# Performance work log

Measured on AMD Instinct MI355X. Metric: run time of the kernel, lower is better.

Reference implementation:

```python
import jax, jax.numpy as jnp
import numpy as np

NUM_BITS = 4
C0, RES0 = 8, 2048
C1, RES1 = 8, 1024
N = 2097152


def _quant_consts(num_bits):
    n = 1 << num_bits
    q = 1.0 / n
    lo = -((n - 1) * 0.5) * q
    hi = n * 0.5 * q
    return n, q, lo, hi


def fake_quant(x, num_bits=NUM_BITS):
    # hard quant path: codes from detached x, dequantize (no grad, matches torch .detach())
    n, q, lo, _ = _quant_consts(num_bits)
    codes = jnp.clip(jnp.round((jax.lax.stop_gradient(x) - lo) / q), 0, n - 1)
    return codes * q + lo


def grid_sample_bilinear(img, gx, gy):
    # img: [C,H,W]; gx,gy: [N] in [-1,1]; align_corners=False, zeros padding
    C, H, W = img.shape
    ix = (gx + 1.0) * 0.5 * W - 0.5
    iy = (gy + 1.0) * 0.5 * H - 0.5
    x0 = jnp.floor(ix)
    y0 = jnp.floor(iy)
    x1, y1 = x0 + 1.0, y0 + 1.0
    wx1 = ix - x0
    wx0 = 1.0 - wx1
    wy1 = iy - y0
    wy0 = 1.0 - wy1

    def tap(xi, yi, w):
        valid = ((xi >= 0) & (xi <= W - 1) & (yi >= 0) & (yi <= H - 1)).astype(img.dtype)
        xc = jnp.clip(xi, 0, W - 1).astype(jnp.int32)
        yc = jnp.clip(yi, 0, H - 1).astype(jnp.int32)
        return img[:, yc, xc] * (valid * w)  # [C,N]

    out = (tap(x0, y0, wx0 * wy0) + tap(x1, y0, wx1 * wy0)
           + tap(x0, y1, wx0 * wy1) + tap(x1, y1, wx1 * wy1))
    return out.T  # [N,C]


def setup_inputs() -> dict:
    key = jax.random.key(0)
    k1, k2, k3 = jax.random.split(key, 3)
    _, _, lo, hi = _quant_consts(NUM_BITS)
    scale = (hi - lo) * 0.25
    uv = jax.random.uniform(k1, (N, 2), dtype=jnp.float32)
    g0 = jax.random.uniform(k2, (1, C0, RES0, RES0), dtype=jnp.float32, minval=-scale, maxval=scale)
    g1 = jax.random.uniform(k3, (1, C1, RES1, RES1), dtype=jnp.float32, minval=-scale, maxval=scale)
    return {"uv": uv, "g0": g0, "g1": g1}


def reference(uv, g0, g1):
    res0 = g0.shape[-1]
    g0q = fake_quant(g0)
    g1q = fake_quant(g1)

    # high-res G0: 4-neighbor gather + concat
    pos = uv * res0 - 0.5
    x0 = jnp.clip(jnp.floor(pos[:, 0]), 0, res0 - 2).astype(jnp.int32)
    y0 = jnp.clip(jnp.floor(pos[:, 1]), 0, res0 - 2).astype(jnp.int32)
    x1, y1 = x0 + 1, y0 + 1
    plane = jnp.transpose(g0q[0], (1, 2, 0))  # [res0, res0, c0]
    feat0 = jnp.concatenate([plane[y0, x0], plane[y0, x1],
                             plane[y1, x0], plane[y1, x1]], axis=-1)  # [N, 4*c0]

    # low-res G1: bilinear grid_sample
    grid = uv * 2.0 - 1.0
    feat1 = grid_sample_bilinear(g1q[0], grid[:, 0], grid[:, 1])  # [N, c1]

    return jnp.concatenate([feat0, feat1], axis=-1)  # [N, 4*c0 + c1]
```

## Files before the change

kernel.cpp:

```cpp
#include <hip/hip_runtime.h>
#include <stdint.h>

#define RES0 2048
#define RES1 1024
#define HW0 (RES0 * RES0)
#define HW1 (RES1 * RES1)

#define QLO (-0.46875f)
#define QSC (0.0625f)

__device__ __forceinline__ uint32_t qcode(float x) {
    float t = (x - QLO) * 16.0f;
    float r = rintf(t);
    r = fminf(fmaxf(r, 0.0f), 15.0f);
    return (uint32_t)(int)r;
}

__device__ __forceinline__ float dq(uint32_t packed, int c) {
    return (float)((packed >> (4 * c)) & 15u) * QSC + QLO;
}

__global__ __launch_bounds__(256) void pack_both_kernel(
    const float4* __restrict__ g0, const float4* __restrict__ g1,
    uint4* __restrict__ p0, uint4* __restrict__ p1)
{
    const int i = blockIdx.x * 256 + threadIdx.x;
    const int n0 = HW0 / 4;
    const int n1 = HW1 / 4;
    if (i < n0) {
        uint4 r = make_uint4(0u, 0u, 0u, 0u);
#pragma unroll
        for (int c = 0; c < 8; ++c) {
            float4 v = g0[(size_t)c * n0 + i];
            r.x |= qcode(v.x) << (4 * c);
            r.y |= qcode(v.y) << (4 * c);
            r.z |= qcode(v.z) << (4 * c);
            r.w |= qcode(v.w) << (4 * c);
        }
        p0[i] = r;
    } else {
        const int j = i - n0;
        if (j < n1) {
            uint4 r = make_uint4(0u, 0u, 0u, 0u);
#pragma unroll
            for (int c = 0; c < 8; ++c) {
                float4 v = g1[(size_t)c * n1 + j];
                r.x |= qcode(v.x) << (4 * c);
                r.y |= qcode(v.y) << (4 * c);
                r.z |= qcode(v.z) << (4 * c);
                r.w |= qcode(v.w) << (4 * c);
            }
            p1[j] = r;
        }
    }
}

__global__ __launch_bounds__(256) void sample_kernel(
    const float2* __restrict__ uv,
    const uint32_t* __restrict__ p0,
    const uint32_t* __restrict__ p1,
    float* __restrict__ out, int n)
{
#pragma clang fp contract(off)
    const int i = blockIdx.x * 256 + threadIdx.x;
    if (i >= n) return;
    const float2 u = uv[i];

    float o[40];

    float px = u.x * 2048.0f; px = px - 0.5f;
    float py = u.y * 2048.0f; py = py - 0.5f;
    float fx = fminf(fmaxf(floorf(px), 0.0f), 2046.0f);
    float fy = fminf(fmaxf(floorf(py), 0.0f), 2046.0f);
    const int x0 = (int)fx;
    const int y0 = (int)fy;
    const uint32_t* row = p0 + y0 * RES0 + x0;
    const uint32_t t00 = row[0];
    const uint32_t t01 = row[1];
    const uint32_t t10 = row[RES0];
    const uint32_t t11 = row[RES0 + 1];
#pragma unroll
    for (int c = 0; c < 8; ++c) {
        o[c]      = dq(t00, c);
        o[8 + c]  = dq(t01, c);
        o[16 + c] = dq(t10, c);
        o[24 + c] = dq(t11, c);
    }

    const float gx = u.x * 2.0f - 1.0f;
    const float gy = u.y * 2.0f - 1.0f;
    float ix = (gx + 1.0f) * 0.5f; ix = ix * 1024.0f; ix = ix - 0.5f;
    float iy = (gy + 1.0f) * 0.5f; iy = iy * 1024.0f; iy = iy - 0.5f;
    const float x0f = floorf(ix);
    const float y0f = floorf(iy);
    const float wx1 = ix - x0f;
    const float wy1 = iy - y0f;
    const float wx0 = 1.0f - wx1;
    const float wy0 = 1.0f - wy1;
    const int jx0 = (int)x0f, jy0 = (int)y0f;
    const int jx1 = jx0 + 1,  jy1 = jy0 + 1;
    const bool vx0 = (jx0 >= 0) && (jx0 <= RES1 - 1);
    const bool vx1 = (jx1 >= 0) && (jx1 <= RES1 - 1);
    const bool vy0 = (jy0 >= 0) && (jy0 <= RES1 - 1);
    const bool vy1 = (jy1 >= 0) && (jy1 <= RES1 - 1);
    const int cx0 = min(max(jx0, 0), RES1 - 1);
    const int cx1 = min(max(jx1, 0), RES1 - 1);
    const int cy0 = min(max(jy0, 0), RES1 - 1);
    const int cy1 = min(max(jy1, 0), RES1 - 1);
    const uint32_t s00 = p1[cy0 * RES1 + cx0];
    const uint32_t s10 = p1[cy0 * RES1 + cx1];
    const uint32_t s01 = p1[cy1 * RES1 + cx0];
    const uint32_t s11 = p1[cy1 * RES1 + cx1];
    const float w00 = (vx0 && vy0) ? wx0 * wy0 : 0.0f;
    const float w10 = (vx1 && vy0) ? wx1 * wy0 : 0.0f;
    const float w01 = (vx0 && vy1) ? wx0 * wy1 : 0.0f;
    const float w11 = (vx1 && vy1) ? wx1 * wy1 : 0.0f;
#pragma unroll
    for (int c = 0; c < 8; ++c) {
        float a = dq(s00, c) * w00 + dq(s10, c) * w10;
        a = a + dq(s01, c) * w01;
        a = a + dq(s11, c) * w11;
        o[32 + c] = a;
    }

    float4* dst = (float4*)(out + (size_t)i * 40);
#pragma unroll
    for (int k = 0; k < 10; ++k) {
        dst[k] = make_float4(o[4 * k], o[4 * k + 1], o[4 * k + 2], o[4 * k + 3]);
    }
}

__device__ __forceinline__ float fq1(float x) {
    float r = fminf(fmaxf(rintf((x - QLO) * 16.0f), 0.0f), 15.0f);
    return r * QSC + QLO;
}

__global__ __launch_bounds__(256) void sample_direct_kernel(
    const float2* __restrict__ uv,
    const float* __restrict__ g0,
    const float* __restrict__ g1,
    float* __restrict__ out, int n)
{
#pragma clang fp contract(off)
    const int i = blockIdx.x * 256 + threadIdx.x;
    if (i >= n) return;
    const float2 u = uv[i];
    float o[40];

    float px = u.x * 2048.0f; px = px - 0.5f;
    float py = u.y * 2048.0f; py = py - 0.5f;
    const int x0 = (int)fminf(fmaxf(floorf(px), 0.0f), 2046.0f);
    const int y0 = (int)fminf(fmaxf(floorf(py), 0.0f), 2046.0f);
#pragma unroll
    for (int c = 0; c < 8; ++c) {
        const float* pl = g0 + (size_t)c * HW0;
        o[c]      = fq1(pl[y0 * RES0 + x0]);
        o[8 + c]  = fq1(pl[y0 * RES0 + x0 + 1]);
        o[16 + c] = fq1(pl[(y0 + 1) * RES0 + x0]);
        o[24 + c] = fq1(pl[(y0 + 1) * RES0 + x0 + 1]);
    }

    const float gx = u.x * 2.0f - 1.0f;
    const float gy = u.y * 2.0f - 1.0f;
    float ix = (gx + 1.0f) * 0.5f; ix = ix * 1024.0f; ix = ix - 0.5f;
    float iy = (gy + 1.0f) * 0.5f; iy = iy * 1024.0f; iy = iy - 0.5f;
    const float x0f = floorf(ix), y0f = floorf(iy);
    const float wx1 = ix - x0f, wy1 = iy - y0f;
    const float wx0 = 1.0f - wx1, wy0 = 1.0f - wy1;
    const int jx0 = (int)x0f, jy0 = (int)y0f;
    const int jx1 = jx0 + 1, jy1 = jy0 + 1;
    const bool vx0 = (jx0 >= 0) && (jx0 < RES1);
    const bool vx1 = (jx1 >= 0) && (jx1 < RES1);
    const bool vy0 = (jy0 >= 0) && (jy0 < RES1);
    const bool vy1 = (jy1 >= 0) && (jy1 < RES1);
    const int cx0 = min(max(jx0, 0), RES1 - 1);
    const int cx1 = min(max(jx1, 0), RES1 - 1);
    const int cy0 = min(max(jy0, 0), RES1 - 1);
    const int cy1 = min(max(jy1, 0), RES1 - 1);
    const float w00 = (vx0 && vy0) ? wx0 * wy0 : 0.0f;
    const float w10 = (vx1 && vy0) ? wx1 * wy0 : 0.0f;
    const float w01 = (vx0 && vy1) ? wx0 * wy1 : 0.0f;
    const float w11 = (vx1 && vy1) ? wx1 * wy1 : 0.0f;
#pragma unroll
    for (int c = 0; c < 8; ++c) {
        const float* pl = g1 + (size_t)c * HW1;
        float a = fq1(pl[cy0 * RES1 + cx0]) * w00 + fq1(pl[cy0 * RES1 + cx1]) * w10;
        a = a + fq1(pl[cy1 * RES1 + cx0]) * w01;
        a = a + fq1(pl[cy1 * RES1 + cx1]) * w11;
        o[32 + c] = a;
    }

    float4* dst = (float4*)(out + (size_t)i * 40);
#pragma unroll
    for (int k = 0; k < 10; ++k) {
        dst[k] = make_float4(o[4 * k], o[4 * k + 1], o[4 * k + 2], o[4 * k + 3]);
    }
}

extern "C" void kernel_launch(void* const* d_in, const int* in_sizes, int n_in,
                              void* d_out, int out_size, void* d_ws, size_t ws_size,
                              hipStream_t stream)
{
    const float* uv = (const float*)d_in[0];
    const float* g0 = (const float*)d_in[1];
    const float* g1 = (const float*)d_in[2];
    float* out = (float*)d_out;
    const int n = in_sizes[0] / 2;

    const size_t need = (size_t)(HW0 + HW1) * sizeof(uint32_t);
    if (ws_size >= need) {
        uint32_t* p0 = (uint32_t*)d_ws;
        uint32_t* p1 = p0 + HW0;
        const int pack_threads = (HW0 + HW1) / 4;
        pack_both_kernel<<<(pack_threads + 255) / 256, 256, 0, stream>>>(
            (const float4*)g0, (const float4*)g1, (uint4*)p0, (uint4*)p1);
        sample_kernel<<<(n + 255) / 256, 256, 0, stream>>>(
            (const float2*)uv, p0, p1, out, n);
    } else {
        sample_direct_kernel<<<(n + 255) / 256, 256, 0, stream>>>(
            (const float2*)uv, g0, g1, out, n);
    }
}
```

Measured before the change: 595.1 us.

## Pack grids into 2x2 texel quads and stage output through LDS for coalesced stores

The packed 4-bit grids are re-laid out so each uint4 holds a 2x2 block of texels, so the four bilinear neighbours of a sample fall within one to four adjacent 16-byte quads, which is meant to improve cache-line locality of the gathers. The sample kernel also writes its 40-float rows into shared memory (padded to 11 float4 per row) and then stores them block-cooperatively, so consecutive threads write consecutive float4s instead of each thread writing a 160-byte strided row. This adds a block barrier, extra LDS traffic and more per-fetch select logic, and the pack kernel now reads float2 with row-pair strides.

```diff
diff --git a/kernel.cpp b/kernel.cpp
--- a/kernel.cpp
+++ b/kernel.cpp
@@ -5,6 +5,8 @@
 #define RES1 1024
 #define HW0 (RES0 * RES0)
 #define HW1 (RES1 * RES1)
+#define NQ0 ((RES0 / 2) * (RES0 / 2))
+#define NQ1 ((RES1 / 2) * (RES1 / 2))
 
 #define QLO (-0.46875f)
 #define QSC (0.0625f)
@@ -20,113 +22,142 @@
     return (float)((packed >> (4 * c)) & 15u) * QSC + QLO;
 }
 
-__global__ __launch_bounds__(256) void pack_both_kernel(
-    const float4* __restrict__ g0, const float4* __restrict__ g1,
-    uint4* __restrict__ p0, uint4* __restrict__ p1)
+__device__ __forceinline__ uint32_t texel_fetch(const uint4* __restrict__ map,
+                                                int pitch_q, int x, int y) {
+    uint4 Q = map[(y >> 1) * pitch_q + (x >> 1)];
+    uint32_t lo = (x & 1) ? Q.y : Q.x;
+    uint32_t hi = (x & 1) ? Q.w : Q.z;
+    return (y & 1) ? hi : lo;
+}
+
+__global__ __launch_bounds__(256) void pack_quads_kernel(
+    const float2* __restrict__ g0, const float2* __restrict__ g1,
+    uint4* __restrict__ q0, uint4* __restrict__ q1)
 {
     const int i = blockIdx.x * 256 + threadIdx.x;
-    const int n0 = HW0 / 4;
-    const int n1 = HW1 / 4;
-    if (i < n0) {
+    if (i < NQ0) {
+        const int qx = i & 1023;
+        const int qy = i >> 10;
         uint4 r = make_uint4(0u, 0u, 0u, 0u);
 #pragma unroll
         for (int c = 0; c < 8; ++c) {
-            float4 v = g0[(size_t)c * n0 + i];
-            r.x |= qcode(v.x) << (4 * c);
-            r.y |= qcode(v.y) << (4 * c);
-            r.z |= qcode(v.z) << (4 * c);
-            r.w |= qcode(v.w) << (4 * c);
-        }
-        p0[i] = r;
+            float2 r0 = g0[(size_t)c * (HW0 / 2) + (size_t)(2 * qy) * 1024 + qx];
+            float2 r1 = g0[(size_t)c * (HW0 / 2) + (size_t)(2 * qy + 1) * 1024 + qx];
+            r.x |= qcode(r0.x) << (4 * c);
+            r.y |= qcode(r0.y) << (4 * c);
+            r.z |= qcode(r1.x) << (4 * c);
+            r.w |= qcode(r1.y) << (4 * c);
+        }
+        q0[i] = r;
     } else {
-        const int j = i - n0;
-        if (j < n1) {
+        const int j = i - NQ0;
+        if (j < NQ1) {
+            const int qx = j & 511;
+            const int qy = j >> 9;
             uint4 r = make_uint4(0u, 0u, 0u, 0u);
 #pragma unroll
             for (int c = 0; c < 8; ++c) {
-                float4 v = g1[(size_t)c * n1 + j];
-                r.x |= qcode(v.x) << (4 * c);
-                r.y |= qcode(v.y) << (4 * c);
-                r.z |= qcode(v.z) << (4 * c);
-                r.w |= qcode(v.w) << (4 * c);
+                float2 r0 = g1[(size_t)c * (HW1 / 2) + (size_t)(2 * qy) * 512 + qx];
+                float2 r1 = g1[(size_t)c * (HW1 / 2) + (size_t)(2 * qy + 1) * 512 + qx];
+                r.x |= qcode(r0.x) << (4 * c);
+                r.y |= qcode(r0.y) << (4 * c);
+                r.z |= qcode(r1.x) << (4 * c);
+                r.w |= qcode(r1.y) << (4 * c);
             }
-            p1[j] = r;
+            q1[j] = r;
         }
     }
 }
 
 __global__ __launch_bounds__(256) void sample_kernel(
     const float2* __restrict__ uv,
-    const uint32_t* __restrict__ p0,
-    const uint32_t* __restrict__ p1,
+    const uint4* __restrict__ q0,
+    const uint4* __restrict__ q1,
     float* __restrict__ out, int n)
 {
 #pragma clang fp contract(off)
-    const int i = blockIdx.x * 256 + threadIdx.x;
-    if (i >= n) return;
-    const float2 u = uv[i];
-
-    float o[40];
-
-    float px = u.x * 2048.0f; px = px - 0.5f;
-    float py = u.y * 2048.0f; py = py - 0.5f;
-    float fx = fminf(fmaxf(floorf(px), 0.0f), 2046.0f);
-    float fy = fminf(fmaxf(floorf(py), 0.0f), 2046.0f);
-    const int x0 = (int)fx;
-    const int y0 = (int)fy;
-    const uint32_t* row = p0 + y0 * RES0 + x0;
-    const uint32_t t00 = row[0];
-    const uint32_t t01 = row[1];
-    const uint32_t t10 = row[RES0];
-    const uint32_t t11 = row[RES0 + 1];
-#pragma unroll
-    for (int c = 0; c < 8; ++c) {
-        o[c]      = dq(t00, c);
-        o[8 + c]  = dq(t01, c);
-        o[16 + c] = dq(t10, c);
-        o[24 + c] = dq(t11, c);
-    }
-
-    const float gx = u.x * 2.0f - 1.0f;
-    const float gy = u.y * 2.0f - 1.0f;
-    float ix = (gx + 1.0f) * 0.5f; ix = ix * 1024.0f; ix = ix - 0.5f;
-    float iy = (gy + 1.0f) * 0.5f; iy = iy * 1024.0f; iy = iy - 0.5f;
-    const float x0f = floorf(ix);
-    const float y0f = floorf(iy);
-    const float wx1 = ix - x0f;
-    const float wy1 = iy - y0f;
-    const float wx0 = 1.0f - wx1;
-    const float wy0 = 1.0f - wy1;
-    const int jx0 = (int)x0f, jy0 = (int)y0f;
-    const int jx1 = jx0 + 1,  jy1 = jy0 + 1;
-    const bool vx0 = (jx0 >= 0) && (jx0 <= RES1 - 1);
-    const bool vx1 = (jx1 >= 0) && (jx1 <= RES1 - 1);
-    const bool vy0 = (jy0 >= 0) && (jy0 <= RES1 - 1);
-    const bool vy1 = (jy1 >= 0) && (jy1 <= RES1 - 1);
-    const int cx0 = min(max(jx0, 0), RES1 - 1);
-    const int cx1 = min(max(jx1, 0), RES1 - 1);
-    const int cy0 = min(max(jy0, 0), RES1 - 1);
-    const int cy1 = min(max(jy1, 0), RES1 - 1);
-    const uint32_t s00 = p1[cy0 * RES1 + cx0];
-    const uint32_t s10 = p1[cy0 * RES1 + cx1];
-    const uint32_t s01 = p1[cy1 * RES1 + cx0];
-    const uint32_t s11 = p1[cy1 * RES1 + cx1];
-    const float w00 = (vx0 && vy0) ? wx0 * wy0 : 0.0f;
-    const float w10 = (vx1 && vy0) ? wx1 * wy0 : 0.0f;
-    const float w01 = (vx0 && vy1) ? wx0 * wy1 : 0.0f;
-    const float w11 = (vx1 && vy1) ? wx1 * wy1 : 0.0f;
-#pragma unroll
-    for (int c = 0; c < 8; ++c) {
-        float a = dq(s00, c) * w00 + dq(s10, c) * w10;
-        a = a + dq(s01, c) * w01;
-        a = a + dq(s11, c) * w11;
-        o[32 + c] = a;
-    }
-
-    float4* dst = (float4*)(out + (size_t)i * 40);
-#pragma unroll
-    for (int k = 0; k < 10; ++k) {
-        dst[k] = make_float4(o[4 * k], o[4 * k + 1], o[4 * k + 2], o[4 * k + 3]);
+    __shared__ float4 lds4[256 * 11];
+    const int t = threadIdx.x;
+    const int i = blockIdx.x * 256 + t;
+
+    if (i < n) {
+        const float2 u = uv[i];
+
+        float px = u.x * 2048.0f; px = px - 0.5f;
+        float py = u.y * 2048.0f; py = py - 0.5f;
+        float fx = fminf(fmaxf(floorf(px), 0.0f), 2046.0f);
+        float fy = fminf(fmaxf(floorf(py), 0.0f), 2046.0f);
+        const int x0 = (int)fx;
+        const int y0 = (int)fy;
+        const uint32_t t00 = texel_fetch(q0, 1024, x0,     y0);
+        const uint32_t t01 = texel_fetch(q0, 1024, x0 + 1, y0);
+        const uint32_t t10 = texel_fetch(q0, 1024, x0,     y0 + 1);
+        const uint32_t t11 = texel_fetch(q0, 1024, x0 + 1, y0 + 1);
+
+        const float gx = u.x * 2.0f - 1.0f;
+        const float gy = u.y * 2.0f - 1.0f;
+        float ix = (gx + 1.0f) * 0.5f; ix = ix * 1024.0f; ix = ix - 0.5f;
+        float iy = (gy + 1.0f) * 0.5f; iy = iy * 1024.0f; iy = iy - 0.5f;
+        const float x0f = floorf(ix);
+        const float y0f = floorf(iy);
+        const float wx1 = ix - x0f;
+        const float wy1 = iy - y0f;
+        const float wx0 = 1.0f - wx1;
+        const float wy0 = 1.0f - wy1;
+        const int jx0 = (int)x0f, jy0 = (int)y0f;
+        const int jx1 = jx0 + 1,  jy1 = jy0 + 1;
+        const bool vx0 = (jx0 >= 0) && (jx0 <= RES1 - 1);
+        const bool vx1 = (jx1 >= 0) && (jx1 <= RES1 - 1);
+        const bool vy0 = (jy0 >= 0) && (jy0 <= RES1 - 1);
+        const bool vy1 = (jy1 >= 0) && (jy1 <= RES1 - 1);
+        const int cx0 = min(max(jx0, 0), RES1 - 1);
+        const int cx1 = min(max(jx1, 0), RES1 - 1);
+        const int cy0 = min(max(jy0, 0), RES1 - 1);
+        const int cy1 = min(max(jy1, 0), RES1 - 1);
+        const uint32_t s00 = texel_fetch(q1, 512, cx0, cy0);
+        const uint32_t s10 = texel_fetch(q1, 512, cx1, cy0);
+        const uint32_t s01 = texel_fetch(q1, 512, cx0, cy1);
+        const uint32_t s11 = texel_fetch(q1, 512, cx1, cy1);
+        const float w00 = (vx0 && vy0) ? wx0 * wy0 : 0.0f;
+        const float w10 = (vx1 && vy0) ? wx1 * wy0 : 0.0f;
+        const float w01 = (vx0 && vy1) ? wx0 * wy1 : 0.0f;
+        const float w11 = (vx1 && vy1) ? wx1 * wy1 : 0.0f;
+
+        float4* my = &lds4[t * 11];
+        my[0] = make_float4(dq(t00, 0), dq(t00, 1), dq(t00, 2), dq(t00, 3));
+        my[1] = make_float4(dq(t00, 4), dq(t00, 5), dq(t00, 6), dq(t00, 7));
+        my[2] = make_float4(dq(t01, 0), dq(t01, 1), dq(t01, 2), dq(t01, 3));
+        my[3] = make_float4(dq(t01, 4), dq(t01, 5), dq(t01, 6), dq(t01, 7));
+        my[4] = make_float4(dq(t10, 0), dq(t10, 1), dq(t10, 2), dq(t10, 3));
+        my[5] = make_float4(dq(t10, 4), dq(t10, 5), dq(t10, 6), dq(t10, 7));
+        my[6] = make_float4(dq(t11, 0), dq(t11, 1), dq(t11, 2), dq(t11, 3));
+        my[7] = make_float4(dq(t11, 4), dq(t11, 5), dq(t11, 6), dq(t11, 7));
+
+        float a[8];
+#pragma unroll
+        for (int c = 0; c < 8; ++c) {
+            float s = dq(s00, c) * w00 + dq(s10, c) * w10;
+            s = s + dq(s01, c) * w01;
+            s = s + dq(s11, c) * w11;
+            a[c] = s;
+        }
+        my[8] = make_float4(a[0], a[1], a[2], a[3]);
+        my[9] = make_float4(a[4], a[5], a[6], a[7]);
+    }
+    __syncthreads();
+
+    const int blk_base = blockIdx.x * 256;
+    const int nblk = min(n - blk_base, 256);
+    const int total = nblk * 10;
+    float4* dst = (float4*)(out + (size_t)blk_base * 40);
+#pragma unroll
+    for (int j = 0; j < 10; ++j) {
+        const int e = j * 256 + t;
+        if (e < total) {
+            const int p = e / 10;
+            const int k = e - p * 10;
+            dst[e] = lds4[p * 11 + k];
+        }
     }
 }
 
@@ -207,15 +238,15 @@
     float* out = (float*)d_out;
     const int n = in_sizes[0] / 2;
 
-    const size_t need = (size_t)(HW0 + HW1) * sizeof(uint32_t);
+    const size_t need = (size_t)(NQ0 + NQ1) * sizeof(uint4);
     if (ws_size >= need) {
-        uint32_t* p0 = (uint32_t*)d_ws;
-        uint32_t* p1 = p0 + HW0;
-        const int pack_threads = (HW0 + HW1) / 4;
-        pack_both_kernel<<<(pack_threads + 255) / 256, 256, 0, stream>>>(
-            (const float4*)g0, (const float4*)g1, (uint4*)p0, (uint4*)p1);
+        uint4* q0 = (uint4*)d_ws;
+        uint4* q1 = q0 + NQ0;
+        const int pack_threads = NQ0 + NQ1;
+        pack_quads_kernel<<<(pack_threads + 255) / 256, 256, 0, stream>>>(
+            (const float2*)g0, (const float2*)g1, q0, q1);
         sample_kernel<<<(n + 255) / 256, 256, 0, stream>>>(
-            (const float2*)uv, p0, p1, out, n);
+            (const float2*)uv, q0, q1, out, n);
     } else {
         sample_direct_kernel<<<(n + 255) / 256, 256, 0, stream>>>(
             (const float2*)uv, g0, g1, out, n);
```

Result: faster. 549.6 us (-7.6%).
